# Kernel optimization log

Hardware: AMD Instinct MI355X
Metric: run time of the kernel (lower is better)

The kernel has to match this reference:

```python
import jax, jax.numpy as jnp
import numpy as np

B, S, D = 64, 512, 768  # batch, max wordpieces (BERT max pos), hidden dim


def setup_inputs() -> dict:
    key = jax.random.key(0)
    k_emb, k_seg = jax.random.split(key)
    # last_hidden_state from the (frozen) BERT backbone
    embeddings = jax.random.normal(k_emb, (B, S, D), dtype=jnp.float32)
    # word-group id per wordpiece token, non-decreasing within each row
    # (token i belongs to word segment_ids[b, i]; '##' continuations share
    #  the id of their head wordpiece, mirroring aggregate_tokens)
    segment_ids = jnp.sort(
        jax.random.randint(k_seg, (B, S), 0, S, dtype=jnp.int32), axis=-1
    )
    return {"embeddings": embeddings, "segment_ids": segment_ids}


def reference(embeddings, segment_ids):
    # Vectorized equivalent of BertEncoder.aggregate_tokens + head slicing:
    # sum wordpiece embeddings within each word group, zero-pad to S words.
    n, s, d = embeddings.shape
    agg = jax.vmap(
        lambda e, seg: jax.ops.segment_sum(e, seg, num_segments=s)
    )(embeddings, segment_ids)  # [B, S, D], trailing unused slots are zeros
    report_feat = agg[:, 0]      # [B, D]   ([CLS] word embedding)
    word_feat = agg[:, 1:]       # [B, S-1, D]
    return report_feat, word_feat
```

## Files before the change

kernel.cpp:

```cpp
#include <hip/hip_runtime.h>


constexpr int B  = 64;
constexpr int S  = 512;
constexpr int D  = 768;
constexpr int D4 = D / 4;
constexpr int BLOCK = 256;

__global__ __launch_bounds__(BLOCK) void segsum_kernel(
    const float4* __restrict__ emb,
    const int*    __restrict__ seg,
    float4*       __restrict__ out) {
  __shared__ int srow[S];

  const int flat = blockIdx.x * BLOCK + threadIdx.x;
  const int b    = flat / (S * D4);

  const int* row = seg + b * S;
  for (int i = threadIdx.x; i < S; i += BLOCK) srow[i] = row[i];
  __syncthreads();

  const int rem = flat - b * (S * D4);
  const int g   = rem / D4;
  const int d4  = rem - g * D4;

  int lo = 0, hi = S;
  while (lo < hi) { int mid = (lo + hi) >> 1; if (srow[mid] < g) lo = mid + 1; else hi = mid; }
  const int start = lo;
  hi = S;
  while (lo < hi) { int mid = (lo + hi) >> 1; if (srow[mid] < g + 1) lo = mid + 1; else hi = mid; }
  const int end = lo;

  float4 acc = make_float4(0.f, 0.f, 0.f, 0.f);
  const float4* p = emb + (size_t)(b * S + start) * D4 + d4;
  for (int s = start; s < end; ++s) {
    float4 e = *p; p += D4;
    acc.x += e.x; acc.y += e.y; acc.z += e.z; acc.w += e.w;
  }

  if (g == 0) {
    out[(size_t)b * D4 + d4] = acc;
  } else {
    out[(size_t)B * D4 + ((size_t)b * (S - 1) + (g - 1)) * D4 + d4] = acc;
  }
}

extern "C" void kernel_launch(void* const* d_in, const int* in_sizes, int n_in,
                              void* d_out, int out_size, void* d_ws, size_t ws_size,
                              hipStream_t stream) {
  const float4* emb = (const float4*)d_in[0];
  const int*    seg = (const int*)d_in[1];
  float4*       out = (float4*)d_out;

  const int total  = B * S * D4;
  const int blocks = total / BLOCK;
  segsum_kernel<<<blocks, BLOCK, 0, stream>>>(emb, seg, out);
}
```

Before: 185.1 us.

## Precompute segment boundaries in a separate kernel and reuse them in segsum

A small pre-pass kernel computes each word group's start offset once per batch row and writes the offsets to workspace. The main kernel then reads start and end from that array instead of staging the segment row in shared memory and running two binary searches per thread. This removes the per-block shared-memory load, the barrier and the search work, at the cost of an extra kernel launch and a workspace round trip. A fallback to the original kernel remains for when the workspace is too small.

```diff
diff --git a/kernel.cpp b/kernel.cpp
--- a/kernel.cpp
+++ b/kernel.cpp
@@ -7,29 +7,35 @@
 constexpr int D4 = D / 4;
 constexpr int BLOCK = 256;
 
-__global__ __launch_bounds__(BLOCK) void segsum_kernel(
+__global__ __launch_bounds__(256) void boundaries_kernel(
+    const int* __restrict__ seg, int* __restrict__ bnd) {
+  __shared__ int srow[S];
+  const int b = blockIdx.x;
+  const int* row = seg + b * S;
+  for (int i = threadIdx.x; i < S; i += 256) srow[i] = row[i];
+  __syncthreads();
+  int* outb = bnd + b * (S + 1);
+  for (int g = threadIdx.x; g < S; g += 256) {
+    int lo = 0, hi = S;
+    while (lo < hi) { int mid = (lo + hi) >> 1; if (srow[mid] < g) lo = mid + 1; else hi = mid; }
+    outb[g] = lo;
+  }
+  if (threadIdx.x == 0) outb[S] = S;
+}
+
+__global__ __launch_bounds__(BLOCK) void segsum_kernel2(
     const float4* __restrict__ emb,
-    const int*    __restrict__ seg,
+    const int*    __restrict__ bnd,
     float4*       __restrict__ out) {
-  __shared__ int srow[S];
-
   const int flat = blockIdx.x * BLOCK + threadIdx.x;
   const int b    = flat / (S * D4);
+  const int rem  = flat - b * (S * D4);
+  const int g    = rem / D4;
+  const int d4   = rem - g * D4;
 
-  const int* row = seg + b * S;
-  for (int i = threadIdx.x; i < S; i += BLOCK) srow[i] = row[i];
-  __syncthreads();
-
-  const int rem = flat - b * (S * D4);
-  const int g   = rem / D4;
-  const int d4  = rem - g * D4;
-
-  int lo = 0, hi = S;
-  while (lo < hi) { int mid = (lo + hi) >> 1; if (srow[mid] < g) lo = mid + 1; else hi = mid; }
-  const int start = lo;
-  hi = S;
-  while (lo < hi) { int mid = (lo + hi) >> 1; if (srow[mid] < g + 1) lo = mid + 1; else hi = mid; }
-  const int end = lo;
+  const int* base  = bnd + b * (S + 1);
+  const int  start = base[g];
+  const int  end   = base[g + 1];
 
   float4 acc = make_float4(0.f, 0.f, 0.f, 0.f);
   const float4* p = emb + (size_t)(b * S + start) * D4 + d4;
@@ -45,6 +51,35 @@
   }
 }
 
+__global__ __launch_bounds__(BLOCK) void segsum_kernel1(
+    const float4* __restrict__ emb,
+    const int*    __restrict__ seg,
+    float4*       __restrict__ out) {
+  __shared__ int srow[S];
+  const int flat = blockIdx.x * BLOCK + threadIdx.x;
+  const int b    = flat / (S * D4);
+  const int* row = seg + b * S;
+  for (int i = threadIdx.x; i < S; i += BLOCK) srow[i] = row[i];
+  __syncthreads();
+  const int rem = flat - b * (S * D4);
+  const int g   = rem / D4;
+  const int d4  = rem - g * D4;
+  int lo = 0, hi = S;
+  while (lo < hi) { int mid = (lo + hi) >> 1; if (srow[mid] < g) lo = mid + 1; else hi = mid; }
+  const int start = lo;
+  hi = S;
+  while (lo < hi) { int mid = (lo + hi) >> 1; if (srow[mid] < g + 1) lo = mid + 1; else hi = mid; }
+  const int end = lo;
+  float4 acc = make_float4(0.f, 0.f, 0.f, 0.f);
+  const float4* p = emb + (size_t)(b * S + start) * D4 + d4;
+  for (int s = start; s < end; ++s) {
+    float4 e = *p; p += D4;
+    acc.x += e.x; acc.y += e.y; acc.z += e.z; acc.w += e.w;
+  }
+  if (g == 0) out[(size_t)b * D4 + d4] = acc;
+  else out[(size_t)B * D4 + ((size_t)b * (S - 1) + (g - 1)) * D4 + d4] = acc;
+}
+
 extern "C" void kernel_launch(void* const* d_in, const int* in_sizes, int n_in,
                               void* d_out, int out_size, void* d_ws, size_t ws_size,
                               hipStream_t stream) {
@@ -54,5 +89,13 @@
 
   const int total  = B * S * D4;
   const int blocks = total / BLOCK;
-  segsum_kernel<<<blocks, BLOCK, 0, stream>>>(emb, seg, out);
+
+  const size_t bnd_bytes = (size_t)B * (S + 1) * sizeof(int);
+  if (ws_size >= bnd_bytes) {
+    int* bnd = (int*)d_ws;
+    boundaries_kernel<<<B, 256, 0, stream>>>(seg, bnd);
+    segsum_kernel2<<<blocks, BLOCK, 0, stream>>>(emb, bnd, out);
+  } else {
+    segsum_kernel1<<<blocks, BLOCK, 0, stream>>>(emb, seg, out);
+  }
 }
```

After: 177.3 us. 1.04x faster.

## Assign one wavefront per segment and find bounds via ballot popcounts

Applied to the files above, without the earlier changes.

Each 64-lane wavefront now owns one (batch, segment) output row, and each lane handles three float4 columns. Segment start and end are found with ballot/popcount counts over int4 loads of the segment-id row, replacing the shared-memory staging, the block barrier and the per-thread binary searches. This drops redundant per-thread search work and LDS traffic, and gives each lane three independent loads per step. In exchange the grid has fewer threads and every wave re-reads the 2KB id row from cache.

```diff
diff --git a/kernel.cpp b/kernel.cpp
--- a/kernel.cpp
+++ b/kernel.cpp
@@ -7,42 +7,54 @@
 constexpr int D4 = D / 4;
 constexpr int BLOCK = 256;
 
-__global__ __launch_bounds__(BLOCK) void segsum_kernel(
+__global__ __launch_bounds__(BLOCK) void segsum_wave_kernel(
     const float4* __restrict__ emb,
     const int*    __restrict__ seg,
     float4*       __restrict__ out) {
-  __shared__ int srow[S];
+  const int wave = (blockIdx.x * BLOCK + threadIdx.x) >> 6;
+  const int lane = threadIdx.x & 63;
+  const int b    = wave >> 9;
+  const int g    = wave & (S - 1);
 
-  const int flat = blockIdx.x * BLOCK + threadIdx.x;
-  const int b    = flat / (S * D4);
+  const int4* row = (const int4*)(seg + b * S);
+  const int4 a0 = row[lane];
+  const int4 a1 = row[lane + 64];
 
-  const int* row = seg + b * S;
-  for (int i = threadIdx.x; i < S; i += BLOCK) srow[i] = row[i];
-  __syncthreads();
+  int start = 0, end = 0;
+  start += __popcll(__ballot(a0.x < g));
+  start += __popcll(__ballot(a0.y < g));
+  start += __popcll(__ballot(a0.z < g));
+  start += __popcll(__ballot(a0.w < g));
+  start += __popcll(__ballot(a1.x < g));
+  start += __popcll(__ballot(a1.y < g));
+  start += __popcll(__ballot(a1.z < g));
+  start += __popcll(__ballot(a1.w < g));
+  end   += __popcll(__ballot(a0.x <= g));
+  end   += __popcll(__ballot(a0.y <= g));
+  end   += __popcll(__ballot(a0.z <= g));
+  end   += __popcll(__ballot(a0.w <= g));
+  end   += __popcll(__ballot(a1.x <= g));
+  end   += __popcll(__ballot(a1.y <= g));
+  end   += __popcll(__ballot(a1.z <= g));
+  end   += __popcll(__ballot(a1.w <= g));
 
-  const int rem = flat - b * (S * D4);
-  const int g   = rem / D4;
-  const int d4  = rem - g * D4;
-
-  int lo = 0, hi = S;
-  while (lo < hi) { int mid = (lo + hi) >> 1; if (srow[mid] < g) lo = mid + 1; else hi = mid; }
-  const int start = lo;
-  hi = S;
-  while (lo < hi) { int mid = (lo + hi) >> 1; if (srow[mid] < g + 1) lo = mid + 1; else hi = mid; }
-  const int end = lo;
-
-  float4 acc = make_float4(0.f, 0.f, 0.f, 0.f);
-  const float4* p = emb + (size_t)(b * S + start) * D4 + d4;
+  float4 acc0 = make_float4(0.f, 0.f, 0.f, 0.f);
+  float4 acc1 = acc0, acc2 = acc0;
+  const float4* p = emb + (size_t)(b * S + start) * D4 + lane;
   for (int s = start; s < end; ++s) {
-    float4 e = *p; p += D4;
-    acc.x += e.x; acc.y += e.y; acc.z += e.z; acc.w += e.w;
+    float4 e0 = p[0], e1 = p[64], e2 = p[128];
+    acc0.x += e0.x; acc0.y += e0.y; acc0.z += e0.z; acc0.w += e0.w;
+    acc1.x += e1.x; acc1.y += e1.y; acc1.z += e1.z; acc1.w += e1.w;
+    acc2.x += e2.x; acc2.y += e2.y; acc2.z += e2.z; acc2.w += e2.w;
+    p += D4;
   }
 
-  if (g == 0) {
-    out[(size_t)b * D4 + d4] = acc;
-  } else {
-    out[(size_t)B * D4 + ((size_t)b * (S - 1) + (g - 1)) * D4 + d4] = acc;
-  }
+  float4* dst = (g == 0)
+      ? out + (size_t)b * D4
+      : out + (size_t)B * D4 + ((size_t)b * (S - 1) + (g - 1)) * D4;
+  dst[lane]       = acc0;
+  dst[lane + 64]  = acc1;
+  dst[lane + 128] = acc2;
 }
 
 extern "C" void kernel_launch(void* const* d_in, const int* in_sizes, int n_in,
@@ -52,7 +64,7 @@
   const int*    seg = (const int*)d_in[1];
   float4*       out = (float4*)d_out;
 
-  const int total  = B * S * D4;
-  const int blocks = total / BLOCK;
-  segsum_kernel<<<blocks, BLOCK, 0, stream>>>(emb, seg, out);
+  const int waves  = B * S;
+  const int blocks = waves / (BLOCK / 64);
+  segsum_wave_kernel<<<blocks, BLOCK, 0, stream>>>(emb, seg, out);
 }
```

After: 176.8 us. -4.5%, faster.
